# Optimization experiments

Hardware: AMD Instinct MI355X
Metric: run time of the kernel (lower is better)

Reference implementation:

```python
import jax, jax.numpy as jnp
import numpy as np

B, C, H, W = 2, 192, 64, 64
HEADS, KS = 6, 7
HD = C // HEADS


def setup_inputs() -> dict:
    key = jax.random.key(0)
    ks = jax.random.split(key, 6)
    s = 0.02
    return {
        "x": jax.random.normal(ks[0], (B, C, H, W), jnp.float32),
        "W_qkv1": jax.random.normal(ks[1], (3 * C, C, 1, 1), jnp.float32) * s,
        "b_qkv1": jnp.zeros((3 * C,), jnp.float32),
        "W_qkv2": jax.random.normal(ks[2], (3 * C, 1, 3, 3), jnp.float32) * s,  # depthwise
        "b_qkv2": jnp.zeros((3 * C,), jnp.float32),
        "temperature": jnp.ones((HEADS, 1, 1, 1), jnp.float32),
        "rpb": jax.random.normal(ks[3], (HEADS, 2 * KS - 1, 2 * KS - 1), jnp.float32) * s,
        "W_proj": jax.random.normal(ks[4], (C, C, 1, 1), jnp.float32) * s,
        "b_proj": jnp.zeros((C,), jnp.float32),
    }


def _conv(x, w, b, pad, groups=1):
    y = jax.lax.conv_general_dilated(
        x, w, (1, 1), pad,
        dimension_numbers=("NCHW", "OIHW", "NCHW"),
        feature_group_count=groups)
    return y + b[None, :, None, None]


def _l2norm(t, eps=1e-12):
    n = jnp.sqrt(jnp.sum(t * t, axis=-1, keepdims=True))
    return t / jnp.maximum(n, eps)


def _nbr_idx(L, K):
    # NATTEN shifted-window neighborhood (dilation=1): window start clamped to image.
    start = jnp.clip(jnp.arange(L) - K // 2, 0, L - K)
    idx = start[:, None] + jnp.arange(K)[None, :]        # [L,K] absolute neighbor index
    rel = idx - jnp.arange(L)[:, None] + (K - 1)         # [L,K] rpb table index
    return idx, rel


def _forward(x, W_qkv1, b_qkv1, W_qkv2, b_qkv2, temperature, rpb, W_proj, b_proj):
    Bq, Cq, Hh, Ww = x.shape
    heads = rpb.shape[0]
    K = (rpb.shape[1] + 1) // 2
    hd = Cq // heads
    qkv = _conv(_conv(x, W_qkv1, b_qkv1, "VALID"), W_qkv2, b_qkv2, "SAME", groups=3 * Cq)
    qkv = qkv.reshape(Bq, 3, heads, hd, Hh, Ww).transpose(1, 0, 2, 4, 5, 3)  # [3,B,h,H,W,d]
    q, k, v = qkv[0], qkv[1], qkv[2]
    q = _l2norm(q)
    k = _l2norm(k)
    idx_i, rel_i = _nbr_idx(Hh, K)
    idx_j, rel_j = _nbr_idx(Ww, K)
    ii = idx_i[:, None, :, None]  # [H,1,K,1]
    jj = idx_j[None, :, None, :]  # [1,W,1,K] -> broadcast [H,W,K,K]
    k_nb = k[:, :, ii, jj, :]     # [B,h,H,W,K,K,d]
    attn = jnp.einsum("bhijd,bhijkld->bhijkl", q, k_nb)
    bias = rpb[:, rel_i[:, None, :, None], rel_j[None, :, None, :]]  # [h,H,W,K,K]
    attn = (attn + bias[None]) * temperature.reshape(1, heads, 1, 1, 1, 1)
    attn = jax.nn.softmax(attn.reshape(Bq, heads, Hh, Ww, K * K), axis=-1)
    v_nb = v[:, :, ii, jj, :].reshape(Bq, heads, Hh, Ww, K * K, hd)
    out = jnp.einsum("bhijk,bhijkd->bhijd", attn, v_nb)
    out = out.transpose(0, 1, 4, 2, 3).reshape(Bq, Cq, Hh, Ww)
    return _conv(out, W_proj, b_proj, "VALID")


def reference(x, W_qkv1, b_qkv1, W_qkv2, b_qkv2, temperature, rpb, W_proj, b_proj):
    return _forward(x, W_qkv1, b_qkv1, W_qkv2, b_qkv2, temperature, rpb, W_proj, b_proj)
```

## Files before the change

### kernel.cpp

```cpp
#include <hip/hip_runtime.h>
#include <math.h>

#define HW 4096

typedef __attribute__((ext_vector_type(8))) short short8;
typedef __attribute__((ext_vector_type(8))) _Float16 half8;
typedef __attribute__((ext_vector_type(4))) float floatx4;

__device__ inline float bflo(unsigned u) { return __uint_as_float(u << 16); }
__device__ inline float bfhi(unsigned u) { return __uint_as_float(u & 0xffff0000u); }
__device__ inline unsigned short f2bf(float x) {
    unsigned u = __float_as_uint(x);
    return (unsigned short)((u + 0x7fffu + ((u >> 16) & 1u)) >> 16);
}
__device__ inline unsigned f2bf2(float lo, float hi) {
    unsigned a = __float_as_uint(lo), b = __float_as_uint(hi);
    a = (a + 0x7fffu + ((a >> 16) & 1u)) >> 16;
    b = (b + 0x7fffu + ((b >> 16) & 1u)) & 0xffff0000u;
    return a | b;
}
__device__ inline unsigned short f2h(float x) {
    _Float16 h = (_Float16)x;
    return __builtin_bit_cast(unsigned short, h);
}


__global__ __launch_bounds__(256) void k_gq(const float* __restrict__ x,
    const float* __restrict__ W1, const float* __restrict__ b1,
    unsigned short* __restrict__ qkv)
{
    __shared__ __align__(16) unsigned short As[64 * 200];
    __shared__ __align__(16) unsigned short Bs[64 * 200];
    const int t = threadIdx.x;
    const int m0 = blockIdx.x * 64;
    const int n0 = blockIdx.y * 64;
    const int w = t >> 6, lane = t & 63;
    const int b = m0 >> 12, px0 = m0 & 4095;
    {
        const float* xb = x + ((size_t)(b * 192) << 12) + px0 + lane;
        const int cb = w * 48;
        #pragma unroll
        for (int r4 = 0; r4 < 12; ++r4) {
            float v0 = xb[(size_t)(cb + r4 * 4 + 0) << 12];
            float v1 = xb[(size_t)(cb + r4 * 4 + 1) << 12];
            float v2 = xb[(size_t)(cb + r4 * 4 + 2) << 12];
            float v3 = xb[(size_t)(cb + r4 * 4 + 3) << 12];
            *(uint2*)&As[lane * 200 + cb + r4 * 4] =
                make_uint2(f2bf2(v0, v1), f2bf2(v2, v3));
        }
    }
    #pragma unroll
    for (int pass = 0; pass < 12; ++pass) {
        int idx = pass * 256 + t;
        int row = idx / 48, ch = idx - row * 48;
        float4 wv = *(const float4*)&W1[(size_t)(n0 + row) * 192 + ch * 4];
        *(uint2*)&Bs[row * 200 + ch * 4] =
            make_uint2(f2bf2(wv.x, wv.y), f2bf2(wv.z, wv.w));
    }
    __syncthreads();
    const int lm = lane & 15, lq = lane >> 4;
    floatx4 acc[4] = {};
    #pragma unroll
    for (int ks = 0; ks < 6; ++ks) {
        short8 bf = *(const short8*)&Bs[(w * 16 + lm) * 200 + ks * 32 + lq * 8];
        #pragma unroll
        for (int mt = 0; mt < 4; ++mt) {
            short8 af = *(const short8*)&As[(mt * 16 + lm) * 200 + ks * 32 + lq * 8];
            acc[mt] = __builtin_amdgcn_mfma_f32_16x16x32_bf16(af, bf, acc[mt], 0, 0, 0);
        }
    }
    __syncthreads();
    const float bias = b1[n0 + w * 16 + lm];
    #pragma unroll
    for (int mt = 0; mt < 4; ++mt)
        #pragma unroll
        for (int r = 0; r < 4; ++r)
            As[(mt * 16 + lq * 4 + r) * 72 + w * 16 + lm] = f2bf(acc[mt][r] + bias);
    __syncthreads();
    #pragma unroll
    for (int pass = 0; pass < 2; ++pass) {
        int idx = pass * 256 + t;
        int m = idx >> 3, n8 = idx & 7;
        uint4 val = *(const uint4*)&As[m * 72 + n8 * 8];
        int oc = n0 + n8 * 8;
        int g = oc >> 5, d = oc & 31;
        *(uint4*)&qkv[((((size_t)(b * 18 + g) << 12) + px0 + m) << 5) + d] = val;
    }
}

__global__ __launch_bounds__(256) void k_dw(const unsigned short* __restrict__ in,
    const float* __restrict__ W2, const float* __restrict__ b2,
    unsigned short* __restrict__ outq)
{
    __shared__ float wsm[288];
    __shared__ float bsm[32];
    const int t = threadIdx.x;
    const int bg = blockIdx.y;
    const int g = (bg >= 18) ? bg - 18 : bg;
    const int cbase = (g / 6) * 192 + (g % 6) * 32;
    for (int idx = t; idx < 288; idx += 256)
        wsm[idx] = W2[(cbase + (idx & 31)) * 9 + (idx >> 5)];
    if (t < 32) bsm[t] = b2[cbase + t];
    __syncthreads();
    const int px = (blockIdx.x << 6) + (t >> 2);
    const int d8 = t & 3;
    const int i = px >> 6, j = px & 63;
    const unsigned short* base = in + ((size_t)bg << 17);
    float acc[8];
    #pragma unroll
    for (int e = 0; e < 8; ++e) acc[e] = bsm[d8 * 8 + e];
    #pragma unroll
    for (int di = -1; di <= 1; ++di) {
        int ii = i + di;
        if (ii < 0 || ii > 63) continue;
        #pragma unroll
        for (int dj = -1; dj <= 1; ++dj) {
            int jj = j + dj;
            if (jj < 0 || jj > 63) continue;
            int tap = (di + 1) * 3 + dj + 1;
            uint4 u = *(const uint4*)(base + ((((ii << 6) + jj) << 5) + d8 * 8));
            const float* wt = &wsm[tap * 32 + d8 * 8];
            acc[0] = fmaf(bflo(u.x), wt[0], acc[0]);
            acc[1] = fmaf(bfhi(u.x), wt[1], acc[1]);
            acc[2] = fmaf(bflo(u.y), wt[2], acc[2]);
            acc[3] = fmaf(bfhi(u.y), wt[3], acc[3]);
            acc[4] = fmaf(bflo(u.z), wt[4], acc[4]);
            acc[5] = fmaf(bfhi(u.z), wt[5], acc[5]);
            acc[6] = fmaf(bflo(u.w), wt[6], acc[6]);
            acc[7] = fmaf(bfhi(u.w), wt[7], acc[7]);
        }
    }
    uint4 o;
    o.x = f2bf2(acc[0], acc[1]); o.y = f2bf2(acc[2], acc[3]);
    o.z = f2bf2(acc[4], acc[5]); o.w = f2bf2(acc[6], acc[7]);
    *(uint4*)(outq + ((size_t)bg << 17) + ((size_t)px << 5) + d8 * 8) = o;
}

__global__ __launch_bounds__(256) void k_attn(const unsigned short* __restrict__ qkv,
    const float* __restrict__ temp, const float* __restrict__ rpb,
    unsigned short* __restrict__ attnO)
{
    __shared__ __align__(16) char lds[45224];
    unsigned short* Ks  = (unsigned short*)lds;
    unsigned short* Ps  = (unsigned short*)lds;
    unsigned short* Vts = (unsigned short*)(lds + 29696);
    float* rpbs = (float*)(lds + 44544);

    const int t = threadIdx.x;
    const int ti = blockIdx.x >> 3, tj = blockIdx.x & 7;
    const int head = blockIdx.y, b = blockIdx.z;
    const int i0 = ti * 8, j0 = tj * 8;
    const int r0 = min(max(i0 - 3, 0), 50), c0 = min(max(j0 - 3, 0), 50);
    const unsigned short* qpl = qkv + ((size_t)(b * 18 + head) << 17);
    const unsigned short* kpl = qkv + ((size_t)(b * 18 + 6 + head) << 17);
    const unsigned short* vpl = qkv + ((size_t)(b * 18 + 12 + head) << 17);

    if (t < 196) {
        int r = (t * 2341) >> 15, cc = t - r * 14;
        int pix = ((r0 + r) << 6) + (c0 + cc);
        const uint4* kg = (const uint4*)(kpl + (pix << 5));
        const uint4* vg = (const uint4*)(vpl + (pix << 5));
        float kf[32];
        float ss = 0.f;
        #pragma unroll
        for (int q = 0; q < 4; ++q) {
            uint4 ku = kg[q];
            unsigned uu[4] = {ku.x, ku.y, ku.z, ku.w};
            #pragma unroll
            for (int e = 0; e < 4; ++e) {
                float lo = bflo(uu[e]), hi = bfhi(uu[e]);
                kf[q * 8 + e * 2] = lo; kf[q * 8 + e * 2 + 1] = hi;
                ss = fmaf(lo, lo, fmaf(hi, hi, ss));
            }
        }
        float rinv = 1.0f / fmaxf(sqrtf(ss), 1e-12f);
        #pragma unroll
        for (int q = 0; q < 4; ++q) {
            uint4 p;
            p.x = f2bf2(kf[q * 8 + 0] * rinv, kf[q * 8 + 1] * rinv);
            p.y = f2bf2(kf[q * 8 + 2] * rinv, kf[q * 8 + 3] * rinv);
            p.z = f2bf2(kf[q * 8 + 4] * rinv, kf[q * 8 + 5] * rinv);
            p.w = f2bf2(kf[q * 8 + 6] * rinv, kf[q * 8 + 7] * rinv);
            *(uint4*)&Ks[t * 40 + q * 8] = p;
        }
        #pragma unroll
        for (int q = 0; q < 4; ++q) {
            uint4 vu = vg[q];
            unsigned uu[4] = {vu.x, vu.y, vu.z, vu.w};
            #pragma unroll
            for (int e = 0; e < 4; ++e) {
                Vts[(q * 8 + e * 2) * 232 + t]     = f2h(bflo(uu[e]));
                Vts[(q * 8 + e * 2 + 1) * 232 + t] = f2h(bfhi(uu[e]));
            }
        }
    }
    for (int idx = t; idx < 448; idx += 256) {
        int row = (idx * 2341) >> 15;
        int c = idx - row * 14;
        ((unsigned*)(Vts + row * 232))[98 + c] = 0u;
    }
    if (t < 169) rpbs[t] = rpb[head * 169 + t];

    const int w = t >> 6, lane = t & 63;
    const int lm = lane & 15, lq = lane >> 4;
    const int px = w * 16 + lm;
    const int i = i0 + (px >> 3), j = j0 + (px & 7);
    uint4 qu = *(const uint4*)(qpl + ((((i << 6) + j) << 5) + lq * 8));
    float qf[8];
    qf[0] = bflo(qu.x); qf[1] = bfhi(qu.x);
    qf[2] = bflo(qu.y); qf[3] = bfhi(qu.y);
    qf[4] = bflo(qu.z); qf[5] = bfhi(qu.z);
    qf[6] = bflo(qu.w); qf[7] = bfhi(qu.w);
    float qs = 0.f;
    #pragma unroll
    for (int e = 0; e < 8; ++e) qs = fmaf(qf[e], qf[e], qs);
    qs += __shfl_xor(qs, 16);
    qs += __shfl_xor(qs, 32);
    float qinv = 1.0f / fmaxf(sqrtf(qs), 1e-12f);
    short8 bq;
    #pragma unroll
    for (int e = 0; e < 8; ++e) bq[e] = (short)f2bf(qf[e] * qinv);
    __syncthreads();

    floatx4 acc[13];
    #pragma unroll
    for (int mt = 0; mt < 13; ++mt) {
        short8 ak = *(const short8*)&Ks[(mt * 16 + lm) * 40 + lq * 8];
        floatx4 z = {0.f, 0.f, 0.f, 0.f};
        acc[mt] = __builtin_amdgcn_mfma_f32_16x16x32_bf16(ak, bq, z, 0, 0, 0);
    }
    __syncthreads();

    const int si = min(max(i - 3, 0), 57), sj = min(max(j - 3, 0), 57);
    const int vloi = si - r0, vloj = sj - c0;
    const int oi = r0 - i + 6, oj = c0 - j + 6;
    const float th = temp[head];
    float mx = -1e30f;
    #pragma unroll
    for (int mt = 0; mt < 13; ++mt) {
        int nb0 = mt * 16 + lq * 4;
        int rh0 = (nb0 * 2341) >> 15;
        int ch0 = nb0 - rh0 * 14;
        #pragma unroll
        for (int r = 0; r < 4; ++r) {
            int ch = ch0 + r, rh = rh0;
            if (ch >= 14) { ch -= 14; rh += 1; }
            int bidx = (rh + oi) * 13 + (ch + oj);
            float bias = rpbs[max(0, min(168, bidx))];
            bool valid = ((unsigned)(rh - vloi) <= 6u) && ((unsigned)(ch - vloj) <= 6u);
            float s = (acc[mt][r] + bias) * th;
            s = valid ? s : -1e30f;
            acc[mt][r] = s;
            mx = fmaxf(mx, s);
        }
    }
    mx = fmaxf(mx, __shfl_xor(mx, 16));
    mx = fmaxf(mx, __shfl_xor(mx, 32));
    float ssum = 0.f;
    #pragma unroll
    for (int mt = 0; mt < 13; ++mt)
        #pragma unroll
        for (int r = 0; r < 4; ++r) {
            float e = __expf(acc[mt][r] - mx);
            acc[mt][r] = e;
            ssum += e;
        }
    ssum += __shfl_xor(ssum, 16);
    ssum += __shfl_xor(ssum, 32);
    const float rs = 1.0f / ssum;

    if (lane < 32) {
        uint4 z4 = {0u, 0u, 0u, 0u};
        *(uint4*)&Ps[(w * 16 + (lane >> 1)) * 232 + 208 + (lane & 1) * 8] = z4;
    }
    #pragma unroll
    for (int mt = 0; mt < 13; ++mt) {
        unsigned lo = (unsigned)f2h(acc[mt][0] * rs) | ((unsigned)f2h(acc[mt][1] * rs) << 16);
        unsigned hi = (unsigned)f2h(acc[mt][2] * rs) | ((unsigned)f2h(acc[mt][3] * rs) << 16);
        *(uint2*)&Ps[px * 232 + mt * 16 + lq * 4] = make_uint2(lo, hi);
    }
    __syncthreads();

    floatx4 oacc[2] = {};
    #pragma unroll
    for (int ks = 0; ks < 7; ++ks) {
        half8 ap = *(const half8*)&Ps[(w * 16 + lm) * 232 + ks * 32 + lq * 8];
        #pragma unroll
        for (int n2 = 0; n2 < 2; ++n2) {
            half8 bv = *(const half8*)&Vts[(n2 * 16 + lm) * 232 + ks * 32 + lq * 8];
            oacc[n2] = __builtin_amdgcn_mfma_f32_16x16x32_f16(ap, bv, oacc[n2], 0, 0, 0);
        }
    }
    #pragma unroll
    for (int n2 = 0; n2 < 2; ++n2)
        #pragma unroll
        for (int r = 0; r < 4; ++r) {
            int p2 = w * 16 + lq * 4 + r;
            int i2 = i0 + (p2 >> 3), j2 = j0 + (p2 & 7);
            attnO[((size_t)((b << 12) + (i2 << 6) + j2)) * 192 + head * 32 + n2 * 16 + lm]
                = f2bf(oacc[n2][r]);
        }
}

__global__ __launch_bounds__(256) void k_gp(const unsigned short* __restrict__ Ain,
    const float* __restrict__ Wp, const float* __restrict__ bp,
    float* __restrict__ out)
{
    __shared__ __align__(16) unsigned short As[64 * 200];
    __shared__ __align__(16) unsigned short Bs[64 * 200];
    const int t = threadIdx.x;
    const int m0 = blockIdx.x * 64;
    const int n0 = blockIdx.y * 64;
    #pragma unroll
    for (int pass = 0; pass < 6; ++pass) {
        int idx = pass * 256 + t;
        int m = idx / 24, c16 = idx % 24;
        *(uint4*)&As[m * 200 + c16 * 8] = *(const uint4*)&Ain[(size_t)(m0 + m) * 192 + c16 * 8];
    }
    #pragma unroll
    for (int pass = 0; pass < 12; ++pass) {
        int idx = pass * 256 + t;
        int row = idx / 48, ch = idx - row * 48;
        float4 wv = *(const float4*)&Wp[(size_t)(n0 + row) * 192 + ch * 4];
        *(uint2*)&Bs[row * 200 + ch * 4] =
            make_uint2(f2bf2(wv.x, wv.y), f2bf2(wv.z, wv.w));
    }
    __syncthreads();
    const int w = t >> 6, lane = t & 63;
    const int lm = lane & 15, lq = lane >> 4;
    floatx4 acc[4] = {};
    #pragma unroll
    for (int ks = 0; ks < 6; ++ks) {
        short8 bf = *(const short8*)&Bs[(w * 16 + lm) * 200 + ks * 32 + lq * 8];
        #pragma unroll
        for (int mt = 0; mt < 4; ++mt) {
            short8 af = *(const short8*)&As[(mt * 16 + lm) * 200 + ks * 32 + lq * 8];
            acc[mt] = __builtin_amdgcn_mfma_f32_16x16x32_bf16(af, bf, acc[mt], 0, 0, 0);
        }
    }
    __syncthreads();
    float* fs = (float*)As;
    const float bias = bp[n0 + w * 16 + lm];
    #pragma unroll
    for (int mt = 0; mt < 4; ++mt)
        #pragma unroll
        for (int r = 0; r < 4; ++r)
            fs[(w * 16 + lm) * 68 + mt * 16 + lq * 4 + r] = acc[mt][r] + bias;
    __syncthreads();
    const int b = m0 >> 12, px0 = m0 & 4095;
    #pragma unroll
    for (int pass = 0; pass < 4; ++pass) {
        int idx = pass * 256 + t;
        int n = idx >> 4, m4 = idx & 15;
        float4 val = *(const float4*)&fs[n * 68 + m4 * 4];
        *(float4*)&out[((size_t)(b * 192 + n0 + n) << 12) + px0 + m4 * 4] = val;
    }
}

extern "C" void kernel_launch(void* const* d_in, const int* in_sizes, int n_in,
                              void* d_out, int out_size, void* d_ws, size_t ws_size,
                              hipStream_t stream) {
    const float* x    = (const float*)d_in[0];
    const float* W1   = (const float*)d_in[1];
    const float* b1   = (const float*)d_in[2];
    const float* W2   = (const float*)d_in[3];
    const float* b2   = (const float*)d_in[4];
    const float* temp = (const float*)d_in[5];
    const float* rpb  = (const float*)d_in[6];
    const float* Wp   = (const float*)d_in[7];
    const float* bp   = (const float*)d_in[8];
    float* out = (float*)d_out;

    char* ws = (char*)d_ws;
    unsigned short* qkv1b = (unsigned short*)(ws);
    unsigned short* qkv2b = (unsigned short*)(ws + 9437184);
    unsigned short* attnO = (unsigned short*)(ws + 18874368);

    k_gq  <<<dim3(128, 9), 256, 0, stream>>>(x, W1, b1, qkv1b);
    k_dw  <<<dim3(64, 36), 256, 0, stream>>>(qkv1b, W2, b2, qkv2b);
    k_attn<<<dim3(64, 6, 2), 256, 0, stream>>>(qkv2b, temp, rpb, attnO);
    k_gp  <<<dim3(128, 3), 256, 0, stream>>>(attnO, Wp, bp, out);
}
```

Baseline: 113.9 us.

## Fuse depthwise 3x3 conv into attention kernel, drop intermediate qkv buffer

Removes the separate depthwise-conv kernel and computes the 3x3 depthwise conv for q, k and v inside the attention kernel, reading the pointwise-conv output directly. This saves a full write and read of the qkv intermediate and one kernel launch. In exchange, the k/v halo (14x14 per 8x8 tile) is recomputed redundantly across neighbouring tiles, each loaded pixel now needs 9 neighbour reads, and register pressure rises from the 32-float accumulators.

Result: no change. 114.8 us (+0.8%).

```diff
diff --git a/kernel.cpp b/kernel.cpp
--- a/kernel.cpp
+++ b/kernel.cpp
@@ -88,67 +88,31 @@
     }
 }
 
-__global__ __launch_bounds__(256) void k_dw(const unsigned short* __restrict__ in,
+__global__ __launch_bounds__(256) void k_attn(const unsigned short* __restrict__ qkv,
     const float* __restrict__ W2, const float* __restrict__ b2,
-    unsigned short* __restrict__ outq)
-{
-    __shared__ float wsm[288];
-    __shared__ float bsm[32];
-    const int t = threadIdx.x;
-    const int bg = blockIdx.y;
-    const int g = (bg >= 18) ? bg - 18 : bg;
-    const int cbase = (g / 6) * 192 + (g % 6) * 32;
-    for (int idx = t; idx < 288; idx += 256)
-        wsm[idx] = W2[(cbase + (idx & 31)) * 9 + (idx >> 5)];
-    if (t < 32) bsm[t] = b2[cbase + t];
-    __syncthreads();
-    const int px = (blockIdx.x << 6) + (t >> 2);
-    const int d8 = t & 3;
-    const int i = px >> 6, j = px & 63;
-    const unsigned short* base = in + ((size_t)bg << 17);
-    float acc[8];
-    #pragma unroll
-    for (int e = 0; e < 8; ++e) acc[e] = bsm[d8 * 8 + e];
-    #pragma unroll
-    for (int di = -1; di <= 1; ++di) {
-        int ii = i + di;
-        if (ii < 0 || ii > 63) continue;
-        #pragma unroll
-        for (int dj = -1; dj <= 1; ++dj) {
-            int jj = j + dj;
-            if (jj < 0 || jj > 63) continue;
-            int tap = (di + 1) * 3 + dj + 1;
-            uint4 u = *(const uint4*)(base + ((((ii << 6) + jj) << 5) + d8 * 8));
-            const float* wt = &wsm[tap * 32 + d8 * 8];
-            acc[0] = fmaf(bflo(u.x), wt[0], acc[0]);
-            acc[1] = fmaf(bfhi(u.x), wt[1], acc[1]);
-            acc[2] = fmaf(bflo(u.y), wt[2], acc[2]);
-            acc[3] = fmaf(bfhi(u.y), wt[3], acc[3]);
-            acc[4] = fmaf(bflo(u.z), wt[4], acc[4]);
-            acc[5] = fmaf(bfhi(u.z), wt[5], acc[5]);
-            acc[6] = fmaf(bflo(u.w), wt[6], acc[6]);
-            acc[7] = fmaf(bfhi(u.w), wt[7], acc[7]);
-        }
-    }
-    uint4 o;
-    o.x = f2bf2(acc[0], acc[1]); o.y = f2bf2(acc[2], acc[3]);
-    o.z = f2bf2(acc[4], acc[5]); o.w = f2bf2(acc[6], acc[7]);
-    *(uint4*)(outq + ((size_t)bg << 17) + ((size_t)px << 5) + d8 * 8) = o;
-}
-
-__global__ __launch_bounds__(256) void k_attn(const unsigned short* __restrict__ qkv,
     const float* __restrict__ temp, const float* __restrict__ rpb,
     unsigned short* __restrict__ attnO)
 {
-    __shared__ __align__(16) char lds[45224];
+    __shared__ __align__(16) char lds[49088];
     unsigned short* Ks  = (unsigned short*)lds;
     unsigned short* Ps  = (unsigned short*)lds;
     unsigned short* Vts = (unsigned short*)(lds + 29696);
     float* rpbs = (float*)(lds + 44544);
+    float* dwW  = (float*)(lds + 45248);
+    float* dwB  = (float*)(lds + 48704);
 
     const int t = threadIdx.x;
+    const int head = blockIdx.y, b = blockIdx.z;
+
+    for (int idx = t; idx < 864; idx += 256) {
+        int plane = idx / 288, rem = idx - plane * 288;
+        dwW[idx] = W2[(plane * 192 + head * 32 + (rem & 31)) * 9 + (rem >> 5)];
+    }
+    if (t < 96) dwB[t] = b2[(t >> 5) * 192 + head * 32 + (t & 31)];
+    if (t < 169) rpbs[t] = rpb[head * 169 + t];
+    __syncthreads();
+
     const int ti = blockIdx.x >> 3, tj = blockIdx.x & 7;
-    const int head = blockIdx.y, b = blockIdx.z;
     const int i0 = ti * 8, j0 = tj * 8;
     const int r0 = min(max(i0 - 3, 0), 50), c0 = min(max(j0 - 3, 0), 50);
     const unsigned short* qpl = qkv + ((size_t)(b * 18 + head) << 17);
@@ -157,60 +121,103 @@
 
     if (t < 196) {
         int r = (t * 2341) >> 15, cc = t - r * 14;
-        int pix = ((r0 + r) << 6) + (c0 + cc);
-        const uint4* kg = (const uint4*)(kpl + (pix << 5));
-        const uint4* vg = (const uint4*)(vpl + (pix << 5));
-        float kf[32];
+        const int pi = r0 + r, pj = c0 + cc;
+        float acc[32];
+        #pragma unroll
+        for (int e = 0; e < 32; ++e) acc[e] = dwB[32 + e];
+        #pragma unroll
+        for (int di = -1; di <= 1; ++di) {
+            int ii = pi + di;
+            if (ii < 0 || ii > 63) continue;
+            #pragma unroll
+            for (int dj = -1; dj <= 1; ++dj) {
+                int jj = pj + dj;
+                if (jj < 0 || jj > 63) continue;
+                const float* wt = &dwW[(9 + (di + 1) * 3 + dj + 1) * 32];
+                const uint4* kg = (const uint4*)(kpl + (((ii << 6) + jj) << 5));
+                #pragma unroll
+                for (int q = 0; q < 4; ++q) {
+                    uint4 u = kg[q];
+                    unsigned uu[4] = {u.x, u.y, u.z, u.w};
+                    #pragma unroll
+                    for (int e = 0; e < 4; ++e) {
+                        acc[q * 8 + e * 2]     = fmaf(bflo(uu[e]), wt[q * 8 + e * 2],     acc[q * 8 + e * 2]);
+                        acc[q * 8 + e * 2 + 1] = fmaf(bfhi(uu[e]), wt[q * 8 + e * 2 + 1], acc[q * 8 + e * 2 + 1]);
+                    }
+                }
+            }
+        }
         float ss = 0.f;
         #pragma unroll
-        for (int q = 0; q < 4; ++q) {
-            uint4 ku = kg[q];
-            unsigned uu[4] = {ku.x, ku.y, ku.z, ku.w};
-            #pragma unroll
-            for (int e = 0; e < 4; ++e) {
-                float lo = bflo(uu[e]), hi = bfhi(uu[e]);
-                kf[q * 8 + e * 2] = lo; kf[q * 8 + e * 2 + 1] = hi;
-                ss = fmaf(lo, lo, fmaf(hi, hi, ss));
-            }
-        }
+        for (int e = 0; e < 32; ++e) ss = fmaf(acc[e], acc[e], ss);
         float rinv = 1.0f / fmaxf(sqrtf(ss), 1e-12f);
         #pragma unroll
         for (int q = 0; q < 4; ++q) {
             uint4 p;
-            p.x = f2bf2(kf[q * 8 + 0] * rinv, kf[q * 8 + 1] * rinv);
-            p.y = f2bf2(kf[q * 8 + 2] * rinv, kf[q * 8 + 3] * rinv);
-            p.z = f2bf2(kf[q * 8 + 4] * rinv, kf[q * 8 + 5] * rinv);
-            p.w = f2bf2(kf[q * 8 + 6] * rinv, kf[q * 8 + 7] * rinv);
+            p.x = f2bf2(acc[q * 8 + 0] * rinv, acc[q * 8 + 1] * rinv);
+            p.y = f2bf2(acc[q * 8 + 2] * rinv, acc[q * 8 + 3] * rinv);
+            p.z = f2bf2(acc[q * 8 + 4] * rinv, acc[q * 8 + 5] * rinv);
+            p.w = f2bf2(acc[q * 8 + 6] * rinv, acc[q * 8 + 7] * rinv);
             *(uint4*)&Ks[t * 40 + q * 8] = p;
         }
         #pragma unroll
-        for (int q = 0; q < 4; ++q) {
-            uint4 vu = vg[q];
-            unsigned uu[4] = {vu.x, vu.y, vu.z, vu.w};
+        for (int e = 0; e < 32; ++e) acc[e] = dwB[64 + e];
+        #pragma unroll
+        for (int di = -1; di <= 1; ++di) {
+            int ii = pi + di;
+            if (ii < 0 || ii > 63) continue;
             #pragma unroll
-            for (int e = 0; e < 4; ++e) {
-                Vts[(q * 8 + e * 2) * 232 + t]     = f2h(bflo(uu[e]));
-                Vts[(q * 8 + e * 2 + 1) * 232 + t] = f2h(bfhi(uu[e]));
+            for (int dj = -1; dj <= 1; ++dj) {
+                int jj = pj + dj;
+                if (jj < 0 || jj > 63) continue;
+                const float* wt = &dwW[(18 + (di + 1) * 3 + dj + 1) * 32];
+                const uint4* vg = (const uint4*)(vpl + (((ii << 6) + jj) << 5));
+                #pragma unroll
+                for (int q = 0; q < 4; ++q) {
+                    uint4 u = vg[q];
+                    unsigned uu[4] = {u.x, u.y, u.z, u.w};
+                    #pragma unroll
+                    for (int e = 0; e < 4; ++e) {
+                        acc[q * 8 + e * 2]     = fmaf(bflo(uu[e]), wt[q * 8 + e * 2],     acc[q * 8 + e * 2]);
+                        acc[q * 8 + e * 2 + 1] = fmaf(bfhi(uu[e]), wt[q * 8 + e * 2 + 1], acc[q * 8 + e * 2 + 1]);
+                    }
+                }
             }
         }
+        #pragma unroll
+        for (int e = 0; e < 32; ++e) Vts[e * 232 + t] = f2h(acc[e]);
     }
     for (int idx = t; idx < 448; idx += 256) {
         int row = (idx * 2341) >> 15;
         int c = idx - row * 14;
         ((unsigned*)(Vts + row * 232))[98 + c] = 0u;
     }
-    if (t < 169) rpbs[t] = rpb[head * 169 + t];
 
     const int w = t >> 6, lane = t & 63;
     const int lm = lane & 15, lq = lane >> 4;
     const int px = w * 16 + lm;
     const int i = i0 + (px >> 3), j = j0 + (px & 7);
-    uint4 qu = *(const uint4*)(qpl + ((((i << 6) + j) << 5) + lq * 8));
     float qf[8];
-    qf[0] = bflo(qu.x); qf[1] = bfhi(qu.x);
-    qf[2] = bflo(qu.y); qf[3] = bfhi(qu.y);
-    qf[4] = bflo(qu.z); qf[5] = bfhi(qu.z);
-    qf[6] = bflo(qu.w); qf[7] = bfhi(qu.w);
+    #pragma unroll
+    for (int e = 0; e < 8; ++e) qf[e] = dwB[lq * 8 + e];
+    #pragma unroll
+    for (int di = -1; di <= 1; ++di) {
+        int ii = i + di;
+        if (ii < 0 || ii > 63) continue;
+        #pragma unroll
+        for (int dj = -1; dj <= 1; ++dj) {
+            int jj = j + dj;
+            if (jj < 0 || jj > 63) continue;
+            const float* wt = &dwW[((di + 1) * 3 + dj + 1) * 32 + lq * 8];
+            uint4 u = *(const uint4*)(qpl + ((((ii << 6) + jj) << 5) + lq * 8));
+            unsigned uu[4] = {u.x, u.y, u.z, u.w};
+            #pragma unroll
+            for (int e = 0; e < 4; ++e) {
+                qf[e * 2]     = fmaf(bflo(uu[e]), wt[e * 2],     qf[e * 2]);
+                qf[e * 2 + 1] = fmaf(bfhi(uu[e]), wt[e * 2 + 1], qf[e * 2 + 1]);
+            }
+        }
+    }
     float qs = 0.f;
     #pragma unroll
     for (int e = 0; e < 8; ++e) qs = fmaf(qf[e], qf[e], qs);
@@ -373,11 +380,9 @@
 
     char* ws = (char*)d_ws;
     unsigned short* qkv1b = (unsigned short*)(ws);
-    unsigned short* qkv2b = (unsigned short*)(ws + 9437184);
-    unsigned short* attnO = (unsigned short*)(ws + 18874368);
+    unsigned short* attnO = (unsigned short*)(ws + 9437184);
 
     k_gq  <<<dim3(128, 9), 256, 0, stream>>>(x, W1, b1, qkv1b);
-    k_dw  <<<dim3(64, 36), 256, 0, stream>>>(qkv1b, W2, b2, qkv2b);
-    k_attn<<<dim3(64, 6, 2), 256, 0, stream>>>(qkv2b, temp, rpb, attnO);
+    k_attn<<<dim3(64, 6, 2), 256, 0, stream>>>(qkv1b, W2, b2, temp, rpb, attnO);
     k_gp  <<<dim3(128, 3), 256, 0, stream>>>(attnO, Wp, bp, out);
 }
```
